# Kernel optimization log

Measured on AMD Instinct MI355X. Metric: run time of the kernel, lower is better.

The kernel has to match this reference:

```python
import jax, jax.numpy as jnp
import numpy as np

H = 4096
IN = 512
OUT = 64


def setup_inputs() -> dict:
    key = jax.random.key(0)
    ks = jax.random.split(key, 10)
    return {
        "inp": jax.random.normal(ks[0], (1, IN), jnp.float32),
        "hidden": jax.random.normal(ks[1], (1, H), jnp.float32),
        "hebb": jax.random.normal(ks[2], (H, H), jnp.float32) * 0.01,
        "W_i2h": jax.random.normal(ks[3], (H, IN), jnp.float32) * (1.0 / np.sqrt(IN)),
        "b_i2h": jax.random.normal(ks[4], (H,), jnp.float32),
        "w": jax.random.uniform(ks[5], (H, H), jnp.float32) * 0.01,
        "plas": jax.random.uniform(ks[6], (H, H), jnp.float32) * 0.01,
        "learn": jnp.full((1,), 0.01, jnp.float32),
        "W_h2o": jax.random.normal(ks[7], (OUT, H), jnp.float32) * (1.0 / np.sqrt(H)),
        "b_h2o": jax.random.normal(ks[8], (OUT,), jnp.float32),
    }


def reference(inp, hidden, hebb, W_i2h, b_i2h, w, plas, learn, W_h2o, b_h2o):
    # plastic-Miconi, rule='hebb', activ='relu'
    # x = relu(i2h(input) + hidden @ (w + plas * hebb))   [1, H]
    pre = inp @ W_i2h.T + b_i2h + hidden @ (w + plas * hebb)
    x = jax.nn.relu(pre)
    # hebb <- (1 - learn) * hebb + learn * outer(hidden, x)   [H, H]
    hebb_new = (1.0 - learn) * hebb + learn * (hidden.T @ x)
    # output = tanh(h2o(x))   [1, OUT]
    out = jnp.tanh(x @ W_h2o.T + b_h2o)
    return out, x, hebb_new
```

## Files before the change

### kernel.cpp

```cpp
#include <hip/hip_runtime.h>
#include <math.h>

#define H 4096
#define INP 512
#define OUTN 64
#define H4 (H / 4)
#define SPLITS 256
#define ROWS_PER_SPLIT (H / SPLITS)

__global__ __launch_bounds__(256) void k_partial(
    const float* __restrict__ hidden,
    const float* __restrict__ w,
    const float* __restrict__ plas,
    const float* __restrict__ hebb,
    float* __restrict__ partial)
{
    const int col4 = blockIdx.x * 256 + threadIdx.x;
    const int i0   = blockIdx.y * ROWS_PER_SPLIT;
    const float4* __restrict__ w4 = (const float4*)w;
    const float4* __restrict__ p4 = (const float4*)plas;
    const float4* __restrict__ h4 = (const float4*)hebb;

    float4 acc = make_float4(0.f, 0.f, 0.f, 0.f);
#pragma unroll 4
    for (int r = 0; r < ROWS_PER_SPLIT; ++r) {
        const int i = i0 + r;
        const float hv = hidden[i];
        const size_t idx = (size_t)i * H4 + col4;
        const float4 wv = w4[idx];
        const float4 pv = p4[idx];
        const float4 hb = h4[idx];
        acc.x += hv * (wv.x + pv.x * hb.x);
        acc.y += hv * (wv.y + pv.y * hb.y);
        acc.z += hv * (wv.z + pv.z * hb.z);
        acc.w += hv * (wv.w + pv.w * hb.w);
    }
    ((float4*)partial)[(size_t)blockIdx.y * H4 + col4] = acc;
}

__global__ __launch_bounds__(256) void k_finish_x(
    const float* __restrict__ partial,
    const float* __restrict__ inp,
    const float* __restrict__ W_i2h,
    const float* __restrict__ b_i2h,
    float* __restrict__ x_out)
{
    const int wave = threadIdx.x >> 6;
    const int lane = threadIdx.x & 63;
    const int j = blockIdx.x * 4 + wave;

    float sum = 0.f;
#pragma unroll
    for (int s = lane; s < SPLITS; s += 64)
        sum += partial[(size_t)s * H + j];

    const float4* __restrict__ row4 = (const float4*)(W_i2h + (size_t)j * INP);
    const float4* __restrict__ in4  = (const float4*)inp;
#pragma unroll
    for (int c = lane; c < INP / 4; c += 64) {
        const float4 a = row4[c];
        const float4 b = in4[c];
        sum += a.x * b.x + a.y * b.y + a.z * b.z + a.w * b.w;
    }
#pragma unroll
    for (int off = 32; off > 0; off >>= 1)
        sum += __shfl_down(sum, off, 64);

    if (lane == 0) {
        const float pre = sum + b_i2h[j];
        x_out[j] = pre > 0.f ? pre : 0.f;
    }
}

__global__ __launch_bounds__(256) void k_hebb(
    const float* __restrict__ hebb,
    const float* __restrict__ hidden,
    const float* __restrict__ x,
    const float* __restrict__ learn,
    float* __restrict__ hebb_out)
{
    const int i = blockIdx.x;
    const float lr = learn[0];
    const float om = 1.f - lr;
    const float coef = lr * hidden[i];
    const float4* __restrict__ hb4 = (const float4*)hebb;
    const float4* __restrict__ x4  = (const float4*)x;
    float4* __restrict__ o4 = (float4*)hebb_out;
    const size_t base = (size_t)i * H4;
#pragma unroll
    for (int c = threadIdx.x; c < H4; c += 256) {
        const float4 h  = hb4[base + c];
        const float4 xv = x4[c];
        float4 r;
        r.x = om * h.x + coef * xv.x;
        r.y = om * h.y + coef * xv.y;
        r.z = om * h.z + coef * xv.z;
        r.w = om * h.w + coef * xv.w;
        o4[base + c] = r;
    }
}

__global__ __launch_bounds__(256) void k_out(
    const float* __restrict__ x,
    const float* __restrict__ W_h2o,
    const float* __restrict__ b_h2o,
    float* __restrict__ out)
{
    const int o = blockIdx.x;
    const float4* __restrict__ row4 = (const float4*)(W_h2o + (size_t)o * H);
    const float4* __restrict__ x4   = (const float4*)x;
    float sum = 0.f;
#pragma unroll
    for (int c = threadIdx.x; c < H4; c += 256) {
        const float4 a = row4[c];
        const float4 b = x4[c];
        sum += a.x * b.x + a.y * b.y + a.z * b.z + a.w * b.w;
    }
#pragma unroll
    for (int off = 32; off > 0; off >>= 1)
        sum += __shfl_down(sum, off, 64);
    __shared__ float red[4];
    const int lane = threadIdx.x & 63;
    const int wave = threadIdx.x >> 6;
    if (lane == 0) red[wave] = sum;
    __syncthreads();
    if (threadIdx.x == 0) {
        const float s = red[0] + red[1] + red[2] + red[3];
        out[o] = tanhf(s + b_h2o[o]);
    }
}

extern "C" void kernel_launch(void* const* d_in, const int* in_sizes, int n_in,
                              void* d_out, int out_size, void* d_ws, size_t ws_size,
                              hipStream_t stream)
{
    const float* inp    = (const float*)d_in[0];
    const float* hidden = (const float*)d_in[1];
    const float* hebb   = (const float*)d_in[2];
    const float* W_i2h  = (const float*)d_in[3];
    const float* b_i2h  = (const float*)d_in[4];
    const float* w      = (const float*)d_in[5];
    const float* plas   = (const float*)d_in[6];
    const float* learn  = (const float*)d_in[7];
    const float* W_h2o  = (const float*)d_in[8];
    const float* b_h2o  = (const float*)d_in[9];

    float* out      = (float*)d_out;
    float* x        = out + OUTN;
    float* hebb_out = x + H;

    const size_t part_bytes = (size_t)SPLITS * H * sizeof(float);
    float* partial = (ws_size >= part_bytes) ? (float*)d_ws : hebb_out;

    k_partial<<<dim3(H / 1024, SPLITS), 256, 0, stream>>>(hidden, w, plas, hebb, partial);
    k_finish_x<<<H / 4, 256, 0, stream>>>(partial, inp, W_i2h, b_i2h, x);
    k_hebb<<<H, 256, 0, stream>>>(hebb, hidden, x, learn, hebb_out);
    k_out<<<OUTN, 256, 0, stream>>>(x, W_h2o, b_h2o, out);
}
```

Before: 263.1 us.

## Use nontemporal loads/stores, double split count, and coalesce partial reduction

The partial matvec now uses 512 row splits, handles two rows per iteration, and loads w and plas with nontemporal hints while hebb stays cached for reuse by the update kernel. The reduction kernel is reorganized so each thread sums a contiguous column across 64 splits, giving coalesced reads, followed by a shared-memory combine. The hebb update is fully unrolled and writes its output with nontemporal stores. Doubling the split count doubles the partial buffer traffic, which may offset some of the gains from the cache hints.

```diff
diff --git a/kernel.cpp b/kernel.cpp
--- a/kernel.cpp
+++ b/kernel.cpp
@@ -5,8 +5,10 @@
 #define INP 512
 #define OUTN 64
 #define H4 (H / 4)
-#define SPLITS 256
-#define ROWS_PER_SPLIT (H / SPLITS)
+#define SPLITS 512
+#define RPS (H / SPLITS)
+
+typedef float fx4 __attribute__((ext_vector_type(4)));
 
 __global__ __launch_bounds__(256) void k_partial(
     const float* __restrict__ hidden,
@@ -16,58 +18,63 @@
     float* __restrict__ partial)
 {
     const int col4 = blockIdx.x * 256 + threadIdx.x;
-    const int i0   = blockIdx.y * ROWS_PER_SPLIT;
-    const float4* __restrict__ w4 = (const float4*)w;
-    const float4* __restrict__ p4 = (const float4*)plas;
-    const float4* __restrict__ h4 = (const float4*)hebb;
+    const int i0   = blockIdx.y * RPS;
+    const fx4* __restrict__ w4 = (const fx4*)w;
+    const fx4* __restrict__ p4 = (const fx4*)plas;
+    const fx4* __restrict__ h4 = (const fx4*)hebb;
 
-    float4 acc = make_float4(0.f, 0.f, 0.f, 0.f);
-#pragma unroll 4
-    for (int r = 0; r < ROWS_PER_SPLIT; ++r) {
-        const int i = i0 + r;
-        const float hv = hidden[i];
-        const size_t idx = (size_t)i * H4 + col4;
-        const float4 wv = w4[idx];
-        const float4 pv = p4[idx];
-        const float4 hb = h4[idx];
-        acc.x += hv * (wv.x + pv.x * hb.x);
-        acc.y += hv * (wv.y + pv.y * hb.y);
-        acc.z += hv * (wv.z + pv.z * hb.z);
-        acc.w += hv * (wv.w + pv.w * hb.w);
+    fx4 acc = (fx4)(0.f);
+    size_t idx = (size_t)i0 * H4 + col4;
+#pragma unroll
+    for (int r = 0; r < RPS; r += 2) {
+        const float hv0 = hidden[i0 + r];
+        const float hv1 = hidden[i0 + r + 1];
+        const fx4 wv0 = __builtin_nontemporal_load(w4 + idx);
+        const fx4 pv0 = __builtin_nontemporal_load(p4 + idx);
+        const fx4 hb0 = h4[idx];
+        const fx4 wv1 = __builtin_nontemporal_load(w4 + idx + H4);
+        const fx4 pv1 = __builtin_nontemporal_load(p4 + idx + H4);
+        const fx4 hb1 = h4[idx + H4];
+        acc += hv0 * (wv0 + pv0 * hb0) + hv1 * (wv1 + pv1 * hb1);
+        idx += 2 * (size_t)H4;
     }
-    ((float4*)partial)[(size_t)blockIdx.y * H4 + col4] = acc;
+    ((fx4*)partial)[(size_t)blockIdx.y * H4 + col4] = acc;
 }
 
-__global__ __launch_bounds__(256) void k_finish_x(
+__global__ __launch_bounds__(256) void k_reduce_x(
     const float* __restrict__ partial,
     const float* __restrict__ inp,
     const float* __restrict__ W_i2h,
     const float* __restrict__ b_i2h,
     float* __restrict__ x_out)
 {
-    const int wave = threadIdx.x >> 6;
-    const int lane = threadIdx.x & 63;
-    const int j = blockIdx.x * 4 + wave;
+    const int jl  = threadIdx.x & 31;
+    const int grp = threadIdx.x >> 5;
+    const int j   = blockIdx.x * 32 + jl;
 
     float sum = 0.f;
+    const float* __restrict__ p = partial + (size_t)grp * 64 * H + j;
+#pragma unroll 8
+    for (int s = 0; s < 64; ++s)
+        sum += p[(size_t)s * H];
+
+    const fx4* __restrict__ row4 = (const fx4*)(W_i2h + (size_t)j * INP);
+    const fx4* __restrict__ in4  = (const fx4*)inp;
 #pragma unroll
-    for (int s = lane; s < SPLITS; s += 64)
-        sum += partial[(size_t)s * H + j];
-
-    const float4* __restrict__ row4 = (const float4*)(W_i2h + (size_t)j * INP);
-    const float4* __restrict__ in4  = (const float4*)inp;
-#pragma unroll
-    for (int c = lane; c < INP / 4; c += 64) {
-        const float4 a = row4[c];
-        const float4 b = in4[c];
+    for (int c = 0; c < 16; ++c) {
+        const fx4 a = row4[grp * 16 + c];
+        const fx4 b = in4[grp * 16 + c];
         sum += a.x * b.x + a.y * b.y + a.z * b.z + a.w * b.w;
     }
+
+    __shared__ float red[8][32];
+    red[grp][jl] = sum;
+    __syncthreads();
+    if (threadIdx.x < 32) {
+        float t = 0.f;
 #pragma unroll
-    for (int off = 32; off > 0; off >>= 1)
-        sum += __shfl_down(sum, off, 64);
-
-    if (lane == 0) {
-        const float pre = sum + b_i2h[j];
+        for (int g = 0; g < 8; ++g) t += red[g][jl];
+        const float pre = t + b_i2h[j];
         x_out[j] = pre > 0.f ? pre : 0.f;
     }
 }
@@ -80,24 +87,26 @@
     float* __restrict__ hebb_out)
 {
     const int i = blockIdx.x;
-    const float lr = learn[0];
-    const float om = 1.f - lr;
+    const float lr   = learn[0];
+    const float om   = 1.f - lr;
     const float coef = lr * hidden[i];
-    const float4* __restrict__ hb4 = (const float4*)hebb;
-    const float4* __restrict__ x4  = (const float4*)x;
-    float4* __restrict__ o4 = (float4*)hebb_out;
-    const size_t base = (size_t)i * H4;
-#pragma unroll
-    for (int c = threadIdx.x; c < H4; c += 256) {
-        const float4 h  = hb4[base + c];
-        const float4 xv = x4[c];
-        float4 r;
-        r.x = om * h.x + coef * xv.x;
-        r.y = om * h.y + coef * xv.y;
-        r.z = om * h.z + coef * xv.z;
-        r.w = om * h.w + coef * xv.w;
-        o4[base + c] = r;
-    }
+    const fx4* __restrict__ hb4 = (const fx4*)hebb + (size_t)i * H4;
+    const fx4* __restrict__ xx4 = (const fx4*)x;
+    fx4* __restrict__ o4 = (fx4*)hebb_out + (size_t)i * H4;
+
+    const int t = threadIdx.x;
+    const fx4 a0 = hb4[t];
+    const fx4 a1 = hb4[t + 256];
+    const fx4 a2 = hb4[t + 512];
+    const fx4 a3 = hb4[t + 768];
+    const fx4 x0 = xx4[t];
+    const fx4 x1 = xx4[t + 256];
+    const fx4 x2 = xx4[t + 512];
+    const fx4 x3 = xx4[t + 768];
+    __builtin_nontemporal_store(om * a0 + coef * x0, o4 + t);
+    __builtin_nontemporal_store(om * a1 + coef * x1, o4 + t + 256);
+    __builtin_nontemporal_store(om * a2 + coef * x2, o4 + t + 512);
+    __builtin_nontemporal_store(om * a3 + coef * x3, o4 + t + 768);
 }
 
 __global__ __launch_bounds__(256) void k_out(
@@ -107,13 +116,13 @@
     float* __restrict__ out)
 {
     const int o = blockIdx.x;
-    const float4* __restrict__ row4 = (const float4*)(W_h2o + (size_t)o * H);
-    const float4* __restrict__ x4   = (const float4*)x;
+    const fx4* __restrict__ row4 = (const fx4*)(W_h2o + (size_t)o * H);
+    const fx4* __restrict__ x4   = (const fx4*)x;
     float sum = 0.f;
 #pragma unroll
     for (int c = threadIdx.x; c < H4; c += 256) {
-        const float4 a = row4[c];
-        const float4 b = x4[c];
+        const fx4 a = row4[c];
+        const fx4 b = x4[c];
         sum += a.x * b.x + a.y * b.y + a.z * b.z + a.w * b.w;
     }
 #pragma unroll
@@ -152,8 +161,8 @@
     const size_t part_bytes = (size_t)SPLITS * H * sizeof(float);
     float* partial = (ws_size >= part_bytes) ? (float*)d_ws : hebb_out;
 
-    k_partial<<<dim3(H / 1024, SPLITS), 256, 0, stream>>>(hidden, w, plas, hebb, partial);
-    k_finish_x<<<H / 4, 256, 0, stream>>>(partial, inp, W_i2h, b_i2h, x);
+    k_partial<<<dim3(H4 / 256, SPLITS), 256, 0, stream>>>(hidden, w, plas, hebb, partial);
+    k_reduce_x<<<H / 32, 256, 0, stream>>>(partial, inp, W_i2h, b_i2h, x);
     k_hebb<<<H, 256, 0, stream>>>(hebb, hidden, x, learn, hebb_out);
     k_out<<<OUTN, 256, 0, stream>>>(x, W_h2o, b_h2o, out);
 }
```

Result: faster. 245.8 us (-6.6%).
